# Kernel tuning notes

Measured on AMD Instinct MI355X. Metric: run time of the kernel, lower is better.

## Reference

```python
import jax, jax.numpy as jnp
import numpy as np

N_NODES = 100000
HIDDEN = 128
N_EDGES = 640000


def setup_inputs() -> dict:
    key = jax.random.key(0)
    ks = jax.random.split(key, 7)
    x = jax.random.normal(ks[0], (N_NODES, HIDDEN), dtype=jnp.float32)
    # torch Linear weights, stored transposed for y = h @ W + b
    W1 = jax.random.normal(ks[1], (HIDDEN, HIDDEN), dtype=jnp.float32) * (1.0 / np.sqrt(HIDDEN))
    b1 = jax.random.normal(ks[2], (HIDDEN,), dtype=jnp.float32) * 0.01
    W2 = jax.random.normal(ks[3], (HIDDEN, 1), dtype=jnp.float32) * (1.0 / np.sqrt(HIDDEN))
    b2 = jax.random.normal(ks[4], (1,), dtype=jnp.float32) * 0.01
    edge_index = jax.random.randint(ks[5], (2, N_EDGES), 0, N_NODES, dtype=jnp.int64 if jax.config.jax_enable_x64 else jnp.int32)
    edge_index_neg = jax.random.randint(ks[6], (2, N_EDGES), 0, N_NODES, dtype=jnp.int64 if jax.config.jax_enable_x64 else jnp.int32)
    return {"x": x, "W1": W1, "b1": b1, "W2": W2, "b2": b2,
            "edge_index": edge_index, "edge_index_neg": edge_index_neg}


def _decode(x, W1, b1, W2, b2, ei):
    # gather endpoints and Hadamard product: [E, hidden]
    h = x[ei[0]] * x[ei[1]]
    # decoder = ReLU -> Linear(h,h) -> ReLU -> Linear(h,1); then sigmoid
    h = jax.nn.relu(h)
    h = jax.nn.relu(h @ W1 + b1)
    return jax.nn.sigmoid(h @ W2 + b2)  # [E, 1]


def reference(x, W1, b1, W2, b2, edge_index, edge_index_neg):
    edge_pos_pred = _decode(x, W1, b1, W2, b2, edge_index)
    edge_neg_pred = _decode(x, W1, b1, W2, b2, edge_index_neg)
    return jnp.concatenate([edge_pos_pred, edge_neg_pred], axis=0)  # [2E, 1]
```

## Files before the change

kernel.cpp:

```cpp
#include <hip/hip_runtime.h>
#include <hip/hip_bf16.h>

#define HID   128
#define PITCH 136
#define TPB   256

typedef __attribute__((ext_vector_type(8))) _Float16 f16x8;
typedef __attribute__((ext_vector_type(8))) __bf16  bf16x8;
typedef __attribute__((ext_vector_type(4))) float   f32x4;

template <int CTRL>
__device__ __forceinline__ float dpp_add(float v) {
  int x = __builtin_bit_cast(int, v);
  int y = __builtin_amdgcn_update_dpp(0, x, CTRL, 0xF, 0xF, true);
  return v + __builtin_bit_cast(float, y);
}

__global__ __launch_bounds__(TPB) void prep_kernel(
    const float* __restrict__ W1, _Float16* __restrict__ w1t,
    const float* __restrict__ x, _Float16* __restrict__ xh, int n_x8) {
  if (xh) {
    for (int i = blockIdx.x * TPB + threadIdx.x; i < n_x8; i += gridDim.x * TPB) {
      float4 a = reinterpret_cast<const float4*>(x)[2 * i];
      float4 b = reinterpret_cast<const float4*>(x)[2 * i + 1];
      f16x8 v;
      v[0] = (_Float16)a.x; v[1] = (_Float16)a.y;
      v[2] = (_Float16)a.z; v[3] = (_Float16)a.w;
      v[4] = (_Float16)b.x; v[5] = (_Float16)b.y;
      v[6] = (_Float16)b.z; v[7] = (_Float16)b.w;
      reinterpret_cast<f16x8*>(xh)[i] = v;
    }
  }
  if (w1t) {
    const int gid = blockIdx.x * TPB + threadIdx.x;
    if (gid < HID * (HID / 8)) {
      const int n  = gid >> 4;
      const int k0 = (gid & 15) << 3;
      f16x8 v;
#pragma unroll
      for (int j = 0; j < 8; ++j) v[j] = (_Float16)W1[(k0 + j) * HID + n];
      *reinterpret_cast<f16x8*>(&w1t[n * HID + k0]) = v;
    }
  }
}

__global__ __launch_bounds__(TPB, 2) void vgae_decode_kernel(
    const _Float16* __restrict__ xh,
    const _Float16* __restrict__ w1t,
    const float* __restrict__ b1,
    const float* __restrict__ W2,
    const float* __restrict__ b2,
    const int* __restrict__ eip,
    const int* __restrict__ ein,
    float* __restrict__ out,
    int E, int n_tiles)
{
  const int lane = threadIdx.x & 63;
  const int wave = threadIdx.x >> 6;
  const int m    = lane & 15;
  const int quad = lane >> 4;
  const float b2v = b2[0];

  f16x8 Bf[8][4];
#pragma unroll
  for (int nt = 0; nt < 8; ++nt)
#pragma unroll
    for (int kt = 0; kt < 4; ++kt)
      Bf[nt][kt] = *reinterpret_cast<const f16x8*>(
          w1t + (nt * 16 + m) * HID + kt * 32 + quad * 8);

  float b1v[8], w2v[8];
#pragma unroll
  for (int nt = 0; nt < 8; ++nt) {
    b1v[nt] = b1[nt * 16 + m];
    w2v[nt] = W2[nt * 16 + m];
  }

  const int stride = gridDim.x;
  const int last   = n_tiles - 1;
  int tile = blockIdx.x;
  if (tile > last) return;

  auto load_idx = [&](int t, int& s, int& d) {
    t = (t > last) ? last : t;
    const int e_base = t * 64 + wave * 16;
    const int* ei = (e_base < E) ? eip : ein;
    const int  eo = (e_base < E) ? e_base : (e_base - E);
    s = ei[eo + m];
    d = ei[E + eo + m];
  };

  f16x8 S[4], D[4];
  {
    int cs, cd;
    load_idx(tile, cs, cd);
    const _Float16* xs = xh + (size_t)cs * HID;
    const _Float16* xd = xh + (size_t)cd * HID;
#pragma unroll
    for (int kt = 0; kt < 4; ++kt) {
      const int k0 = kt * 32 + quad * 8;
      S[kt] = *reinterpret_cast<const f16x8*>(xs + k0);
      D[kt] = *reinterpret_cast<const f16x8*>(xd + k0);
    }
  }
  int ns, nd;
  load_idx(tile + stride, ns, nd);

  const f16x8 zero8 = (f16x8)(_Float16)0;

  for (; tile <= last; tile += stride) {
    const _Float16* nxs = xh + (size_t)ns * HID;
    const _Float16* nxd = xh + (size_t)nd * HID;
    load_idx(tile + 2 * stride, ns, nd);

    f16x8 a[4];
#pragma unroll
    for (int kt = 0; kt < 4; ++kt) {
      f16x8 pr = S[kt] * D[kt];
      a[kt] = __builtin_elementwise_max(pr, zero8);
    }

#pragma unroll
    for (int kt = 0; kt < 4; ++kt) {
      const int k0 = kt * 32 + quad * 8;
      S[kt] = *reinterpret_cast<const f16x8*>(nxs + k0);
      D[kt] = *reinterpret_cast<const f16x8*>(nxd + k0);
    }

    f32x4 acc[8];
#pragma unroll
    for (int nt = 0; nt < 8; ++nt) {
      f32x4 t;
      t[0] = b1v[nt]; t[1] = b1v[nt]; t[2] = b1v[nt]; t[3] = b1v[nt];
      acc[nt] = t;
    }

    __builtin_amdgcn_s_setprio(1);
#pragma unroll
    for (int kt = 0; kt < 4; ++kt)
#pragma unroll
      for (int nt = 0; nt < 8; ++nt)
        acc[nt] = __builtin_amdgcn_mfma_f32_16x16x32_f16(a[kt], Bf[nt][kt], acc[nt], 0, 0, 0);
    __builtin_amdgcn_s_setprio(0);

    float p[4] = {0.f, 0.f, 0.f, 0.f};
#pragma unroll
    for (int nt = 0; nt < 8; ++nt) {
#pragma unroll
      for (int r = 0; r < 4; ++r)
        p[r] = fmaf(fmaxf(acc[nt][r], 0.f), w2v[nt], p[r]);
    }
#pragma unroll
    for (int r = 0; r < 4; ++r) {
      p[r] = dpp_add<0xB1>(p[r]);
      p[r] = dpp_add<0x4E>(p[r]);
      p[r] = dpp_add<0x124>(p[r]);
      p[r] = dpp_add<0x128>(p[r]);
    }
    if (m == 0) {
      float4 o;
      o.x = 1.f / (1.f + __expf(-(p[0] + b2v)));
      o.y = 1.f / (1.f + __expf(-(p[1] + b2v)));
      o.z = 1.f / (1.f + __expf(-(p[2] + b2v)));
      o.w = 1.f / (1.f + __expf(-(p[3] + b2v)));
      *reinterpret_cast<float4*>(out + tile * 64 + wave * 16 + quad * 4) = o;
    }
  }
}

__global__ __launch_bounds__(TPB) void vgae_decode_fallback(
    const float* __restrict__ x,
    const float* __restrict__ W1,
    const float* __restrict__ b1,
    const float* __restrict__ W2,
    const float* __restrict__ b2,
    const int* __restrict__ eip,
    const int* __restrict__ ein,
    float* __restrict__ out,
    int E, int n_tiles)
{
  __shared__ __bf16 sW[HID * PITCH];
  __shared__ float  sb1[HID];
  __shared__ float  sw2[HID];
  for (int c = threadIdx.x; c < HID * (HID / 8); c += TPB) {
    int n = c >> 4, k0 = (c & 15) << 3;
    bf16x8 v;
#pragma unroll
    for (int j = 0; j < 8; ++j) v[j] = (__bf16)W1[(k0 + j) * HID + n];
    *reinterpret_cast<bf16x8*>(&sW[n * PITCH + k0]) = v;
  }
  if (threadIdx.x < HID) { sb1[threadIdx.x] = b1[threadIdx.x]; sw2[threadIdx.x] = W2[threadIdx.x]; }
  __syncthreads();
  const int lane = threadIdx.x & 63, wave = threadIdx.x >> 6;
  const int m = lane & 15, quad = lane >> 4;
  const float b2v = b2[0];
  for (int tile = blockIdx.x; tile < n_tiles; tile += gridDim.x) {
    const int e_base = tile * 64 + wave * 16;
    const int* ei = (e_base < E) ? eip : ein;
    const int  eo = (e_base < E) ? e_base : (e_base - E);
    const int src = ei[eo + m], dst = ei[E + eo + m];
    const float* xs = x + (size_t)src * HID;
    const float* xd = x + (size_t)dst * HID;
    f32x4 acc[8] = {};
#pragma unroll
    for (int kt = 0; kt < 4; ++kt) {
      const int k0 = kt * 32 + quad * 8;
      float4 s0 = *reinterpret_cast<const float4*>(xs + k0);
      float4 s1 = *reinterpret_cast<const float4*>(xs + k0 + 4);
      float4 d0 = *reinterpret_cast<const float4*>(xd + k0);
      float4 d1 = *reinterpret_cast<const float4*>(xd + k0 + 4);
      bf16x8 a;
      a[0] = (__bf16)fmaxf(s0.x * d0.x, 0.f); a[1] = (__bf16)fmaxf(s0.y * d0.y, 0.f);
      a[2] = (__bf16)fmaxf(s0.z * d0.z, 0.f); a[3] = (__bf16)fmaxf(s0.w * d0.w, 0.f);
      a[4] = (__bf16)fmaxf(s1.x * d1.x, 0.f); a[5] = (__bf16)fmaxf(s1.y * d1.y, 0.f);
      a[6] = (__bf16)fmaxf(s1.z * d1.z, 0.f); a[7] = (__bf16)fmaxf(s1.w * d1.w, 0.f);
#pragma unroll
      for (int nt = 0; nt < 8; ++nt) {
        bf16x8 bfr = *reinterpret_cast<const bf16x8*>(&sW[(nt * 16 + m) * PITCH + k0]);
        acc[nt] = __builtin_amdgcn_mfma_f32_16x16x32_bf16(a, bfr, acc[nt], 0, 0, 0);
      }
    }
    float p[4] = {0.f, 0.f, 0.f, 0.f};
#pragma unroll
    for (int nt = 0; nt < 8; ++nt) {
      const int n = nt * 16 + m;
      const float b1n = sb1[n], w2n = sw2[n];
#pragma unroll
      for (int r = 0; r < 4; ++r) p[r] = fmaf(fmaxf(acc[nt][r] + b1n, 0.f), w2n, p[r]);
    }
#pragma unroll
    for (int off = 1; off < 16; off <<= 1)
#pragma unroll
      for (int r = 0; r < 4; ++r) p[r] += __shfl_xor(p[r], off, 64);
    if (m == 0) {
      float4 o;
      o.x = 1.f / (1.f + __expf(-(p[0] + b2v)));
      o.y = 1.f / (1.f + __expf(-(p[1] + b2v)));
      o.z = 1.f / (1.f + __expf(-(p[2] + b2v)));
      o.w = 1.f / (1.f + __expf(-(p[3] + b2v)));
      *reinterpret_cast<float4*>(out + tile * 64 + wave * 16 + quad * 4) = o;
    }
  }
}

extern "C" void kernel_launch(void* const* d_in, const int* in_sizes, int n_in,
                              void* d_out, int out_size, void* d_ws, size_t ws_size,
                              hipStream_t stream) {
  const float* x  = (const float*)d_in[0];
  const float* W1 = (const float*)d_in[1];
  const float* b1 = (const float*)d_in[2];
  const float* W2 = (const float*)d_in[3];
  const float* b2 = (const float*)d_in[4];
  const int*  eip = (const int*)d_in[5];
  const int*  ein = (const int*)d_in[6];
  float* out = (float*)d_out;
  const int E = in_sizes[5] / 2;
  const int n_tiles = (2 * E) / 64;
  const int n_nodes = in_sizes[0] / HID;
  const int n_x8 = in_sizes[0] / 8;

  const size_t w1t_bytes = (size_t)HID * HID * sizeof(_Float16);
  const size_t xh_off    = 65536;
  const size_t xh_bytes  = (size_t)n_nodes * HID * sizeof(_Float16);

  _Float16* w1t = nullptr;
  _Float16* xh  = nullptr;
  if (ws_size >= w1t_bytes) w1t = (_Float16*)d_ws;
  if (ws_size >= xh_off + xh_bytes) xh = (_Float16*)((char*)d_ws + xh_off);

  if (w1t && xh) {
    int prep_grid = (n_x8 + TPB - 1) / TPB;
    if (prep_grid > 6400) prep_grid = 6400;
    prep_kernel<<<prep_grid, TPB, 0, stream>>>(W1, w1t, x, xh, n_x8);
    vgae_decode_kernel<<<512, TPB, 0, stream>>>(xh, w1t, b1, W2, b2,
                                                eip, ein, out, E, n_tiles);
  } else {
    vgae_decode_fallback<<<2560, TPB, 0, stream>>>(x, W1, b1, W2, b2,
                                                   eip, ein, out, E, n_tiles);
  }
}
```

Baseline: 190.7 us.

## Fuse prep and decode into one cooperative kernel with grid sync

Merges the fp16 cast/transpose prep kernel and the decode kernel into a single cooperative launch, separated by a grid-wide barrier. This removes one kernel launch and the gap between the two kernels. In exchange, the cast phase now runs on only 512 blocks instead of up to 6400, and every block waits at the grid sync. If the cooperative launch fails, the code falls back to the old two-kernel path.

```diff
diff --git a/kernel.cpp b/kernel.cpp
--- a/kernel.cpp
+++ b/kernel.cpp
@@ -1,9 +1,13 @@
 #include <hip/hip_runtime.h>
+#include <hip/hip_cooperative_groups.h>
 #include <hip/hip_bf16.h>
+
+namespace cg = cooperative_groups;
 
 #define HID   128
 #define PITCH 136
 #define TPB   256
+#define DEC_GRID 512
 
 typedef __attribute__((ext_vector_type(8))) _Float16 f16x8;
 typedef __attribute__((ext_vector_type(8))) __bf16  bf16x8;
@@ -16,43 +20,39 @@
   return v + __builtin_bit_cast(float, y);
 }
 
-__global__ __launch_bounds__(TPB) void prep_kernel(
-    const float* __restrict__ W1, _Float16* __restrict__ w1t,
-    const float* __restrict__ x, _Float16* __restrict__ xh, int n_x8) {
-  if (xh) {
-    for (int i = blockIdx.x * TPB + threadIdx.x; i < n_x8; i += gridDim.x * TPB) {
-      float4 a = reinterpret_cast<const float4*>(x)[2 * i];
-      float4 b = reinterpret_cast<const float4*>(x)[2 * i + 1];
-      f16x8 v;
-      v[0] = (_Float16)a.x; v[1] = (_Float16)a.y;
-      v[2] = (_Float16)a.z; v[3] = (_Float16)a.w;
-      v[4] = (_Float16)b.x; v[5] = (_Float16)b.y;
-      v[6] = (_Float16)b.z; v[7] = (_Float16)b.w;
-      reinterpret_cast<f16x8*>(xh)[i] = v;
-    }
-  }
-  if (w1t) {
-    const int gid = blockIdx.x * TPB + threadIdx.x;
-    if (gid < HID * (HID / 8)) {
-      const int n  = gid >> 4;
-      const int k0 = (gid & 15) << 3;
-      f16x8 v;
-#pragma unroll
-      for (int j = 0; j < 8; ++j) v[j] = (_Float16)W1[(k0 + j) * HID + n];
-      *reinterpret_cast<f16x8*>(&w1t[n * HID + k0]) = v;
-    }
-  }
-}
-
-__global__ __launch_bounds__(TPB, 2) void vgae_decode_kernel(
-    const _Float16* __restrict__ xh,
-    const _Float16* __restrict__ w1t,
-    const float* __restrict__ b1,
-    const float* __restrict__ W2,
-    const float* __restrict__ b2,
-    const int* __restrict__ eip,
-    const int* __restrict__ ein,
-    float* __restrict__ out,
+__device__ __forceinline__ void cast_phase(const float* __restrict__ x,
+                                           _Float16* __restrict__ xh,
+                                           int n_x8, int gid, int gsz) {
+  for (int i = gid; i < n_x8; i += gsz) {
+    float4 a = reinterpret_cast<const float4*>(x)[2 * i];
+    float4 b = reinterpret_cast<const float4*>(x)[2 * i + 1];
+    f16x8 v;
+    v[0] = (_Float16)a.x; v[1] = (_Float16)a.y;
+    v[2] = (_Float16)a.z; v[3] = (_Float16)a.w;
+    v[4] = (_Float16)b.x; v[5] = (_Float16)b.y;
+    v[6] = (_Float16)b.z; v[7] = (_Float16)b.w;
+    reinterpret_cast<f16x8*>(xh)[i] = v;
+  }
+}
+
+__device__ __forceinline__ void transpose_phase(const float* __restrict__ W1,
+                                                _Float16* __restrict__ w1t,
+                                                int gid) {
+  if (gid < HID * (HID / 8)) {
+    const int n  = gid >> 4;
+    const int k0 = (gid & 15) << 3;
+    f16x8 v;
+#pragma unroll
+    for (int j = 0; j < 8; ++j) v[j] = (_Float16)W1[(k0 + j) * HID + n];
+    *reinterpret_cast<f16x8*>(&w1t[n * HID + k0]) = v;
+  }
+}
+
+__device__ __forceinline__ void decode_phase(
+    const _Float16* __restrict__ xh, const _Float16* __restrict__ w1t,
+    const float* __restrict__ b1, const float* __restrict__ W2,
+    const float* __restrict__ b2, const int* __restrict__ eip,
+    const int* __restrict__ ein, float* __restrict__ out,
     int E, int n_tiles)
 {
   const int lane = threadIdx.x & 63;
@@ -166,6 +166,39 @@
       *reinterpret_cast<float4*>(out + tile * 64 + wave * 16 + quad * 4) = o;
     }
   }
+}
+
+__global__ __launch_bounds__(TPB, 2) void vgae_fused_kernel(
+    const float* __restrict__ x, const float* __restrict__ W1,
+    const float* __restrict__ b1, const float* __restrict__ W2,
+    const float* __restrict__ b2, const int* __restrict__ eip,
+    const int* __restrict__ ein, float* __restrict__ out,
+    int E, int n_tiles, _Float16* __restrict__ xh,
+    _Float16* __restrict__ w1t, int n_x8)
+{
+  const int gid = blockIdx.x * TPB + threadIdx.x;
+  cast_phase(x, xh, n_x8, gid, gridDim.x * TPB);
+  transpose_phase(W1, w1t, gid);
+  cg::this_grid().sync();
+  decode_phase(xh, w1t, b1, W2, b2, eip, ein, out, E, n_tiles);
+}
+
+__global__ __launch_bounds__(TPB) void prep_kernel(
+    const float* __restrict__ W1, _Float16* __restrict__ w1t,
+    const float* __restrict__ x, _Float16* __restrict__ xh, int n_x8) {
+  const int gid = blockIdx.x * TPB + threadIdx.x;
+  if (xh) cast_phase(x, xh, n_x8, gid, gridDim.x * TPB);
+  if (w1t) transpose_phase(W1, w1t, gid);
+}
+
+__global__ __launch_bounds__(TPB, 2) void vgae_decode_kernel(
+    const _Float16* __restrict__ xh, const _Float16* __restrict__ w1t,
+    const float* __restrict__ b1, const float* __restrict__ W2,
+    const float* __restrict__ b2, const int* __restrict__ eip,
+    const int* __restrict__ ein, float* __restrict__ out,
+    int E, int n_tiles)
+{
+  decode_phase(xh, w1t, b1, W2, b2, eip, ein, out, E, n_tiles);
 }
 
 __global__ __launch_bounds__(TPB) void vgae_decode_fallback(
@@ -254,10 +287,10 @@
   const int*  eip = (const int*)d_in[5];
   const int*  ein = (const int*)d_in[6];
   float* out = (float*)d_out;
-  const int E = in_sizes[5] / 2;
-  const int n_tiles = (2 * E) / 64;
+  int E = in_sizes[5] / 2;
+  int n_tiles = (2 * E) / 64;
   const int n_nodes = in_sizes[0] / HID;
-  const int n_x8 = in_sizes[0] / 8;
+  int n_x8 = in_sizes[0] / 8;
 
   const size_t w1t_bytes = (size_t)HID * HID * sizeof(_Float16);
   const size_t xh_off    = 65536;
@@ -269,11 +302,22 @@
   if (ws_size >= xh_off + xh_bytes) xh = (_Float16*)((char*)d_ws + xh_off);
 
   if (w1t && xh) {
-    int prep_grid = (n_x8 + TPB - 1) / TPB;
-    if (prep_grid > 6400) prep_grid = 6400;
-    prep_kernel<<<prep_grid, TPB, 0, stream>>>(W1, w1t, x, xh, n_x8);
-    vgae_decode_kernel<<<512, TPB, 0, stream>>>(xh, w1t, b1, W2, b2,
-                                                eip, ein, out, E, n_tiles);
+    void* kargs[] = {
+      (void*)&x, (void*)&W1, (void*)&b1, (void*)&W2, (void*)&b2,
+      (void*)&eip, (void*)&ein, (void*)&out,
+      (void*)&E, (void*)&n_tiles, (void*)&xh, (void*)&w1t, (void*)&n_x8
+    };
+    hipError_t err = hipLaunchCooperativeKernel(
+        (const void*)vgae_fused_kernel, dim3(DEC_GRID), dim3(TPB),
+        kargs, 0, stream);
+    if (err != hipSuccess) {
+      (void)hipGetLastError();
+      int prep_grid = (n_x8 + TPB - 1) / TPB;
+      if (prep_grid > 6400) prep_grid = 6400;
+      prep_kernel<<<prep_grid, TPB, 0, stream>>>(W1, w1t, x, xh, n_x8);
+      vgae_decode_kernel<<<DEC_GRID, TPB, 0, stream>>>(xh, w1t, b1, W2, b2,
+                                                       eip, ein, out, E, n_tiles);
+    }
   } else {
     vgae_decode_fallback<<<2560, TPB, 0, stream>>>(x, W1, b1, W2, b2,
                                                    eip, ein, out, E, n_tiles);
```

After: 270.6 us. 1.42x slower.
